# Performance work log

Measured on AMD Instinct MI355X. Metric: run time of the kernel, lower is better.

The kernel has to match this reference:

```python
import jax, jax.numpy as jnp
import numpy as np


def _mlp1(x, W, b):
    return jax.nn.relu(x @ W + b)


def _forward(battle_x, side_x, user_x, moveset_feat, movepool_feat, lookup_move_feat,
             lookup_move_mask, lastberry, lastberry_mask, items, abilities, types_x,
             tera_types_x, opt_moves, move_mask, can_tera, switch_mask,
             W_item, b_item, W_ab, b_ab, W_ms, b_ms, W_user, b_user,
             W_mo1, b_mo1, W_mo2, b_mo2, W_so1, b_so1, W_so2, b_so2,
             active_idx, switch_idx):
    B = battle_x.shape[0]
    # --- user block (vectorized over [B, 2 sides, 6 team members]) ---
    ms = _mlp1(moveset_feat, W_ms, b_ms)                    # [B,2,6,4,128]
    pool = _mlp1(movepool_feat, W_ms, b_ms).mean(axis=-2)   # [B,2,6,128] mean over move pool
    move_set_x = jnp.maximum(ms.max(axis=-2), pool)         # max over [4 slots + pool-mean]
    item_x = _mlp1(items, W_item, b_item).mean(axis=-2)     # [B,2,6,128]
    ability_x = _mlp1(abilities, W_ab, b_ab).mean(axis=-2)  # [B,2,6,128]
    # optional lookup slots: mask*relu(Wx+b) == zero vector when absent
    lk = _mlp1(lookup_move_feat, W_ms, b_ms) * lookup_move_mask[..., None]  # [B,2,6,5,128]
    berry = _mlp1(lastberry, W_item, b_item) * lastberry_mask[..., None]    # [B,2,6,128]
    lk_flat = lk.reshape(B, 2, 6, 5 * 128)
    u_in = jnp.concatenate([user_x, lk_flat, berry, move_set_x, item_x, ability_x,
                            types_x, tera_types_x], axis=-1)                # [B,2,6,1281]
    u = _mlp1(u_in, W_user, b_user)                                         # [B,2,6,512]
    # --- side block ---
    active = jnp.take_along_axis(u, active_idx[:, :, None, None], axis=2)[:, :, 0]  # [B,2,512]
    side_out = jnp.concatenate([side_x, active, u.max(axis=2)], axis=-1)    # [B,2,1041]
    battle_full = jnp.concatenate([battle_x, side_out[:, 0], side_out[:, 1]], axis=-1)  # [B,2091]
    D = battle_full.shape[-1]
    # --- move options: 4 moves x tera in {0,1} ---
    bt = jnp.broadcast_to(battle_full[:, None, None, :], (B, 4, 2, D))
    mv = jnp.broadcast_to(opt_moves[:, :, None, :], (B, 4, 2, 128))
    tera = jnp.broadcast_to(jnp.arange(2, dtype=battle_x.dtype)[None, None, :, None], (B, 4, 2, 1))
    xm = jnp.concatenate([bt, mv, tera], axis=-1)                           # [B,4,2,2220]
    mlogit = (_mlp1(xm, W_mo1, b_mo1) @ W_mo2 + b_mo2)[..., 0]              # [B,4,2]
    tera_ok = jnp.stack([jnp.ones_like(can_tera), can_tera], axis=-1)       # [B,2]
    mvalid = move_mask[:, :, None] * tera_ok[:, None, :]
    mlogit = jnp.where(mvalid > 0, mlogit, -jnp.inf).reshape(B, 8)
    # --- switch options ---
    sw = jnp.take_along_axis(u[:, 0], switch_idx[:, :, None], axis=1)       # [B,6,512]
    xs = jnp.concatenate([jnp.broadcast_to(battle_full[:, None, :], (B, 6, D)), sw], axis=-1)
    slogit = (_mlp1(xs, W_so1, b_so1) @ W_so2 + b_so2)[..., 0]              # [B,6]
    slogit = jnp.where(switch_mask > 0, slogit, -jnp.inf)
    return jnp.concatenate([mlogit, slogit], axis=-1)                       # [B,14]


def setup_inputs() -> dict:
    key = jax.random.key(0)
    ks = jax.random.split(key, 40)
    B = 512
    f32 = jnp.float32
    n = lambda k, s, sc=1.0: jax.random.normal(k, s, f32) * sc
    bern = lambda k, s, p: (jax.random.uniform(k, s) < p).astype(f32)
    inp = {
        'battle_x': n(ks[0], (B, 9)),
        'side_x': n(ks[1], (B, 2, 17)),
        'user_x': n(ks[2], (B, 2, 6, 89)),
        'moveset_feat': n(ks[3], (B, 2, 6, 4, 516)),
        'movepool_feat': n(ks[4], (B, 2, 6, 8, 516)),
        'lookup_move_feat': n(ks[5], (B, 2, 6, 5, 516)),
        'lookup_move_mask': bern(ks[6], (B, 2, 6, 5), 0.5),
        'lastberry': n(ks[7], (B, 2, 6, 256)),
        'lastberry_mask': bern(ks[8], (B, 2, 6), 0.5),
        'items': n(ks[9], (B, 2, 6, 2, 256)),
        'abilities': n(ks[10], (B, 2, 6, 2, 256)),
        'types_x': bern(ks[11], (B, 2, 6, 20), 0.1),
        'tera_types_x': bern(ks[12], (B, 2, 6, 20), 0.1),
        'opt_moves': n(ks[13], (B, 4, 128)),
        'move_mask': bern(ks[14], (B, 4), 0.9),
        'can_tera': bern(ks[15], (B,), 0.5),
        'switch_mask': bern(ks[16], (B, 6), 0.8),
        'W_item': n(ks[17], (256, 128), 0.05), 'b_item': n(ks[18], (128,), 0.05),
        'W_ab': n(ks[19], (256, 128), 0.05), 'b_ab': n(ks[20], (128,), 0.05),
        'W_ms': n(ks[21], (516, 128), 0.05), 'b_ms': n(ks[22], (128,), 0.05),
        'W_user': n(ks[23], (1281, 512), 0.02), 'b_user': n(ks[24], (512,), 0.02),
        'W_mo1': n(ks[25], (2220, 512), 0.02), 'b_mo1': n(ks[26], (512,), 0.02),
        'W_mo2': n(ks[27], (512, 1), 0.05), 'b_mo2': n(ks[28], (1,), 0.05),
        'W_so1': n(ks[29], (2603, 512), 0.02), 'b_so1': n(ks[30], (512,), 0.02),
        'W_so2': n(ks[31], (512, 1), 0.05), 'b_so2': n(ks[32], (1,), 0.05),
        'active_idx': jax.random.randint(ks[33], (B, 2), 0, 6),
        'switch_idx': jax.random.randint(ks[34], (B, 6), 0, 6),
    }
    return inp


def reference(battle_x, side_x, user_x, moveset_feat, movepool_feat, lookup_move_feat,
              lookup_move_mask, lastberry, lastberry_mask, items, abilities, types_x,
              tera_types_x, opt_moves, move_mask, can_tera, switch_mask,
              W_item, b_item, W_ab, b_ab, W_ms, b_ms, W_user, b_user,
              W_mo1, b_mo1, W_mo2, b_mo2, W_so1, b_so1, W_so2, b_so2,
              active_idx, switch_idx):
    return _forward(battle_x, side_x, user_x, moveset_feat, movepool_feat, lookup_move_feat,
                    lookup_move_mask, lastberry, lastberry_mask, items, abilities, types_x,
                    tera_types_x, opt_moves, move_mask, can_tera, switch_mask,
                    W_item, b_item, W_ab, b_ab, W_ms, b_ms, W_user, b_user,
                    W_mo1, b_mo1, W_mo2, b_mo2, W_so1, b_so1, W_so2, b_so2,
                    active_idx, switch_idx)
```

## Files before the change

kernel.cpp:

```cpp
#include <hip/hip_runtime.h>
#include <math.h>

#define BATCH 512
#define NEG_BIG (-3.0e38f)

typedef __attribute__((ext_vector_type(8))) short short8;
typedef __attribute__((ext_vector_type(4))) float floatx4;

__device__ inline unsigned pk2(float lo, float hi) {
    return __builtin_amdgcn_perm(__float_as_uint(hi), __float_as_uint(lo), 0x07060302u);
}
__device__ inline short8 cvt8(float4 a, float4 b) {
    union { unsigned u[4]; short8 s; } r;
    r.u[0] = pk2(a.x, a.y); r.u[1] = pk2(a.z, a.w);
    r.u[2] = pk2(b.x, b.y); r.u[3] = pk2(b.z, b.w);
    return r.s;
}
__device__ inline short f2bf(float f) {
    unsigned u = __float_as_uint(f);
    u += 0x7FFFu + ((u >> 16) & 1u);
    return (short)(u >> 16);
}
__device__ inline float bf2f(short s) {
    return __uint_as_float(((unsigned)(unsigned short)s) << 16);
}

__device__ inline void wprep_body(
    const float* __restrict__ W, int K, int N,
    short* __restrict__ Wt, int KP, int k_off,
    int lid, int kbt, float (*tile)[33])
{
    const int kb = (lid % kbt) * 32, nb = (lid / kbt) * 32;
    const int c = threadIdx.x & 31, r0 = threadIdx.x >> 5;
    #pragma unroll
    for (int i = 0; i < 4; ++i) {
        const int r = r0 + i * 8;
        const int k = kb + r;
        tile[r][c] = (k < K) ? W[(size_t)k * N + nb + c] : 0.f;
    }
    __syncthreads();
    #pragma unroll
    for (int i = 0; i < 4; ++i) {
        const int n = nb + r0 + i * 8;
        Wt[(size_t)n * KP + k_off + kb + c] = f2bf(tile[c][r0 + i * 8]);
    }
}

__global__ __launch_bounds__(256) void k_wprep_all(
    const float* __restrict__ W_ms, const float* __restrict__ W_item,
    const float* __restrict__ W_ab, const float* __restrict__ W_user,
    const float* __restrict__ W_mo1, const float* __restrict__ W_so1,
    short* __restrict__ Wt_pre, short* __restrict__ Wt_user,
    short* __restrict__ Wt_mo, short* __restrict__ Wt_mv,
    short* __restrict__ Wt_so, short* __restrict__ Wt_sw)
{
    __shared__ float tile[32][33];
    const int l = blockIdx.x;
    if      (l < 68)   wprep_body(W_ms,   516,  128, Wt_pre,  1056, 0,   l,        17, tile);
    else if (l < 100)  wprep_body(W_item, 256,  128, Wt_pre,  1056, 544, l - 68,   8,  tile);
    else if (l < 132)  wprep_body(W_ab,   256,  128, Wt_pre,  1056, 800, l - 100,  8,  tile);
    else if (l < 788)  wprep_body(W_user, 1281, 512, Wt_user, 1312, 0,   l - 132,  41, tile);
    else if (l < 1844) wprep_body(W_mo1,  2091, 512, Wt_mo,   2112, 0,   l - 788,  66, tile);
    else if (l < 1908) wprep_body(W_mo1 + (size_t)2091 * 512, 128, 512, Wt_mv, 128, 0, l - 1844, 4, tile);
    else if (l < 2964) wprep_body(W_so1,  2091, 512, Wt_so,   2112, 0,   l - 1908, 66, tile);
    else               wprep_body(W_so1 + (size_t)2091 * 512, 512, 512, Wt_sw, 512, 0, l - 2964, 16, tile);
}

#define STRA 552
#define SIOFF 18768
#define STRI 264
#define ZEROE 528

__device__ inline void stage4(short* S, int e, float4 v) {
    uint2 wv; wv.x = pk2(v.x, v.y); wv.y = pk2(v.z, v.w);
    *(uint2*)(S + e) = wv;
}

__global__ __launch_bounds__(256, 3) void k_pre_gemm(
    const float* __restrict__ moveset, const float* __restrict__ movepool,
    const float* __restrict__ lookup,  const float* __restrict__ items,
    const float* __restrict__ lastberry, const float* __restrict__ abilities,
    const float* __restrict__ lookup_mask, const float* __restrict__ berry_mask,
    const float* __restrict__ user_x, const float* __restrict__ types_x,
    const float* __restrict__ tera_types,
    const short* __restrict__ Wt,
    const float* __restrict__ b_ms, const float* __restrict__ b_item,
    const float* __restrict__ b_ab,
    short* __restrict__ u_in)
{
    __shared__ __align__(16) short S[21408];
    const int t = threadIdx.x;
    const int bsu0 = blockIdx.x * 2;

    {
        #pragma unroll
        for (int j = 0; j < 2; ++j) {
            const int i = t + j * 256;
            if (i < 476) {
                const int rr = i / 14, p = i - rr * 14;
                *(unsigned*)(S + rr * STRA + 516 + p * 2) = 0u;
            }
        }

        const float4* msrc = (const float4*)(moveset + (size_t)bsu0 * 4 * 516);
        const float4* psrc = (const float4*)(movepool + (size_t)bsu0 * 8 * 516);
        const float4* lsrc = (const float4*)(lookup + (size_t)bsu0 * 5 * 516);
        const float4* isrc = (const float4*)(items + (size_t)bsu0 * 2 * 256);
        const float4* bsrc = (const float4*)(lastberry + (size_t)bsu0 * 256);
        const float4* asrc = (const float4*)(abilities + (size_t)bsu0 * 2 * 256);

        float4 rm[5], rp[9], rl[6], rit, rlb, rab;
        #pragma unroll
        for (int j = 0; j < 5; ++j) {
            int i = t + j * 256; if (i > 1031) i = 1031;
            rm[j] = msrc[i];
        }
        #pragma unroll
        for (int j = 0; j < 9; ++j) {
            int i = t + j * 256; if (i > 2063) i = 2063;
            rp[j] = psrc[i];
        }
        #pragma unroll
        for (int j = 0; j < 6; ++j) {
            int i = t + j * 256; if (i > 1289) i = 1289;
            rl[j] = lsrc[i];
        }
        rit = isrc[t];
        rlb = bsrc[t & 127];
        rab = asrc[t];

        __builtin_amdgcn_sched_barrier(0);

        #pragma unroll
        for (int j = 0; j < 5; ++j) {
            int i = t + j * 256; if (i > 1031) i = 1031;
            const int g = i / 129, jj = i - g * 129;
            stage4(S, ((g >> 2) * 17 + (g & 3)) * STRA + jj * 4, rm[j]);
        }
        #pragma unroll
        for (int j = 0; j < 9; ++j) {
            int i = t + j * 256; if (i > 2063) i = 2063;
            const int g = i / 129, jj = i - g * 129;
            stage4(S, ((g >> 3) * 17 + 4 + (g & 7)) * STRA + jj * 4, rp[j]);
        }
        #pragma unroll
        for (int j = 0; j < 6; ++j) {
            int i = t + j * 256; if (i > 1289) i = 1289;
            const int g = i / 129, jj = i - g * 129;
            const int b = g / 5, r = g - b * 5;
            stage4(S, (b * 17 + 12 + r) * STRA + jj * 4, rl[j]);
        }
        {
            const int g = t >> 6, j = t & 63;
            stage4(S, SIOFF + ((g >> 1) * 5 + (g & 1)) * STRI + j * 4, rit);
        }
        {
            const int i = t & 127, g = i >> 6, j = i & 63;
            stage4(S, SIOFF + (g * 5 + 2) * STRI + j * 4, rlb);
        }
        {
            const int g = t >> 6, j = t & 63;
            stage4(S, SIOFF + ((g >> 1) * 5 + 3 + (g & 1)) * STRI + j * 4, rab);
        }
    }
    __syncthreads();

    const int lane = t & 63, w = t >> 6;
    const int m = lane & 15, q = lane >> 4;

    int t2base = ZEROE, t2lo = 1, t2hi = 0;
    {
        int jj = m, b = 0;
        if (m >= 6 && m < 12) { b = 1; jj = m - 6; }
        if (m < 12) {
            if (jj == 0)      { t2base = (b * 17 + 16) * STRA;             t2lo = 0;  t2hi = 16; }
            else if (jj <= 2) { t2base = SIOFF + (b * 5 + (jj - 1)) * STRI; t2lo = 17; t2hi = 24; }
            else if (jj == 3) { t2base = SIOFF + (b * 5 + 2) * STRI;        t2lo = 17; t2hi = 24; }
            else              { t2base = SIOFF + (b * 5 + 3 + (jj - 4)) * STRI; t2lo = 25; t2hi = 32; }
        }
    }
    const short* bp0 = Wt + (size_t)(w * 32 + m) * 1056 + q * 8;
    const short* bp1 = bp0 + (size_t)16 * 1056;

    floatx4 acc[3][2];
    #pragma unroll
    for (int i = 0; i < 3; ++i) {
        acc[i][0] = (floatx4){0.f, 0.f, 0.f, 0.f};
        acc[i][1] = (floatx4){0.f, 0.f, 0.f, 0.f};
    }

    short8 B0[4], B1[4];
    #pragma unroll
    for (int d = 0; d < 4; ++d) {
        B0[d] = *(const short8*)(bp0 + d * 32);
        B1[d] = *(const short8*)(bp1 + d * 32);
    }
    const int aoff = q * 8;

    #pragma unroll
    for (int s = 0; s <= 16; ++s) {
        const int k0 = s * 32 + aoff;
        short8 a0 = *(const short8*)(S + m * STRA + k0);
        short8 a1 = *(const short8*)(S + (17 + m) * STRA + k0);
        const int e2 = (s >= t2lo && s <= t2hi) ? t2base + (s - t2lo) * 32 + aoff : ZEROE;
        short8 a2 = *(const short8*)(S + e2);
        acc[0][0] = __builtin_amdgcn_mfma_f32_16x16x32_bf16(a0, B0[s & 3], acc[0][0], 0, 0, 0);
        acc[0][1] = __builtin_amdgcn_mfma_f32_16x16x32_bf16(a0, B1[s & 3], acc[0][1], 0, 0, 0);
        acc[1][0] = __builtin_amdgcn_mfma_f32_16x16x32_bf16(a1, B0[s & 3], acc[1][0], 0, 0, 0);
        acc[1][1] = __builtin_amdgcn_mfma_f32_16x16x32_bf16(a1, B1[s & 3], acc[1][1], 0, 0, 0);
        acc[2][0] = __builtin_amdgcn_mfma_f32_16x16x32_bf16(a2, B0[s & 3], acc[2][0], 0, 0, 0);
        acc[2][1] = __builtin_amdgcn_mfma_f32_16x16x32_bf16(a2, B1[s & 3], acc[2][1], 0, 0, 0);
        if (s + 4 <= 32) {
            B0[s & 3] = *(const short8*)(bp0 + (s + 4) * 32);
            B1[s & 3] = *(const short8*)(bp1 + (s + 4) * 32);
        }
    }
    #pragma unroll
    for (int s = 17; s <= 32; ++s) {
        const int e2 = (s >= t2lo && s <= t2hi) ? t2base + (s - t2lo) * 32 + aoff : ZEROE;
        short8 a2 = *(const short8*)(S + e2);
        acc[2][0] = __builtin_amdgcn_mfma_f32_16x16x32_bf16(a2, B0[s & 3], acc[2][0], 0, 0, 0);
        acc[2][1] = __builtin_amdgcn_mfma_f32_16x16x32_bf16(a2, B1[s & 3], acc[2][1], 0, 0, 0);
        if (s + 4 <= 32) {
            B0[s & 3] = *(const short8*)(bp0 + (s + 4) * 32);
            B1[s & 3] = *(const short8*)(bp1 + (s + 4) * 32);
        }
    }

    __syncthreads();
    float* ec = (float*)S;

    #pragma unroll
    for (int nt = 0; nt < 2; ++nt) {
        const int col = w * 32 + nt * 16 + m;
        #pragma unroll
        for (int r = 0; r < 4; ++r) {
            const int row = q * 4 + r;
            ec[col * 49 + row]      = acc[0][nt][r];
            ec[col * 49 + 24 + row] = acc[1][nt][r];
            if (row < 6)            ec[col * 49 + 16 + row]            = acc[2][nt][r];
            else if (row < 12)      ec[col * 49 + 24 + 16 + (row - 6)] = acc[2][nt][r];
        }
    }
    __syncthreads();
    {
        const int c  = t & 127;
        const int bi = t >> 7;
        const int bsu = bsu0 + bi;
        const float* v = &ec[c * 49 + bi * 24];
        short* __restrict__ orow = u_in + (size_t)bsu * 1312;
        const float bms = b_ms[c], bit = b_item[c], bab = b_ab[c];
        float msx = 0.f;
        #pragma unroll
        for (int r = 0; r < 4; ++r) msx = fmaxf(msx, v[r] + bms);
        float pool = 0.f;
        #pragma unroll
        for (int r = 4; r < 12; ++r) pool += fmaxf(v[r] + bms, 0.f);
        pool *= 0.125f;
        orow[857 + c] = f2bf(fmaxf(msx, pool));
        #pragma unroll
        for (int sl = 0; sl < 5; ++sl) {
            const float mask = lookup_mask[bsu * 5 + sl];
            orow[89 + sl * 128 + c] = f2bf(fmaxf(v[12 + sl] + bms, 0.f) * mask);
        }
        orow[985 + c]  = f2bf(0.5f * (fmaxf(v[17] + bit, 0.f) + fmaxf(v[18] + bit, 0.f)));
        orow[729 + c]  = f2bf(fmaxf(v[19] + bit, 0.f) * berry_mask[bsu]);
        orow[1113 + c] = f2bf(0.5f * (fmaxf(v[20] + bab, 0.f) + fmaxf(v[21] + bab, 0.f)));
        if (c < 89) orow[c] = f2bf(user_x[(size_t)bsu * 89 + c]);
        if (c < 20) {
            orow[1241 + c] = f2bf(types_x[bsu * 20 + c]);
            orow[1261 + c] = f2bf(tera_types[bsu * 20 + c]);
        }
        if (c < 31) orow[1281 + c] = 0;
    }
}

template<int AMODE, bool ABF16, bool RELU, bool HASBIAS, bool OBF16>
__global__ __launch_bounds__(256, 3) void k_gemm(
    const void* __restrict__ Av, int strideA,
    const void* __restrict__ gbasev, const int* __restrict__ gidx,
    const short* __restrict__ Wt, int KP,
    const float* __restrict__ bias,
    void* __restrict__ Cv, size_t partStride, int ksteps)
{
    const int t = threadIdx.x, lane = t & 63, w = t >> 6;
    const int m = lane & 15, q = lane >> 4;
    const int bid = blockIdx.y * gridDim.x + blockIdx.x;
    const int mb = (bid / gridDim.y) * 32;
    const int nb = (bid % gridDim.y) * 128 + w * 32;
    const int z = blockIdx.z;
    const int koff = z * ksteps * 32;

    const short* aps[2]; const float* apf[2];
    #pragma unroll
    for (int i = 0; i < 2; ++i) {
        const int row = mb + i * 16 + m;
        size_t roff;
        if (AMODE == 0) roff = (size_t)row * strideA;
        else {
            const int bb = row / 6, j = row - bb * 6;
            roff = ((size_t)bb * 12 + gidx[bb * 6 + j]) * 512;
        }
        if (ABF16) aps[i] = (const short*)Av + roff + koff + q * 8;
        else       apf[i] = (const float*)Av + roff + koff + q * 8;
        if (AMODE == 1) aps[i] = (const short*)gbasev + roff + koff + q * 8;
    }
    const short* bp0 = Wt + (size_t)(nb + m) * KP + koff + q * 8;
    const short* bp1 = bp0 + (size_t)16 * KP;

    floatx4 acc[2][2];
    #pragma unroll
    for (int i = 0; i < 2; ++i) {
        acc[i][0] = (floatx4){0.f, 0.f, 0.f, 0.f};
        acc[i][1] = (floatx4){0.f, 0.f, 0.f, 0.f};
    }

    short8 Ab[4][2];
    float4 Af[4][2][2];
    short8 B0b[4], B1b[4];
    #pragma unroll
    for (int d = 0; d < 4; ++d) {
        #pragma unroll
        for (int i = 0; i < 2; ++i) {
            if (ABF16) Ab[d][i] = *(const short8*)(aps[i] + d * 32);
            else {
                Af[d][i][0] = *(const float4*)(apf[i] + d * 32);
                Af[d][i][1] = *(const float4*)(apf[i] + d * 32 + 4);
            }
        }
        B0b[d] = *(const short8*)(bp0 + d * 32);
        B1b[d] = *(const short8*)(bp1 + d * 32);
    }

    int s = 0;
    for (; s + 4 < ksteps; s += 4) {
        #pragma unroll
        for (int d = 0; d < 4; ++d) {
            #pragma unroll
            for (int i = 0; i < 2; ++i) {
                const short8 av = ABF16 ? Ab[d][i] : cvt8(Af[d][i][0], Af[d][i][1]);
                acc[i][0] = __builtin_amdgcn_mfma_f32_16x16x32_bf16(av, B0b[d], acc[i][0], 0, 0, 0);
                acc[i][1] = __builtin_amdgcn_mfma_f32_16x16x32_bf16(av, B1b[d], acc[i][1], 0, 0, 0);
            }
            int ns = s + d + 4; if (ns > ksteps - 1) ns = ksteps - 1;
            const int o = ns * 32;
            #pragma unroll
            for (int i = 0; i < 2; ++i) {
                if (ABF16) Ab[d][i] = *(const short8*)(aps[i] + o);
                else {
                    Af[d][i][0] = *(const float4*)(apf[i] + o);
                    Af[d][i][1] = *(const float4*)(apf[i] + o + 4);
                }
            }
            B0b[d] = *(const short8*)(bp0 + o);
            B1b[d] = *(const short8*)(bp1 + o);
        }
    }
    #pragma unroll
    for (int d = 0; d < 4; ++d) {
        if (s + d < ksteps) {
            #pragma unroll
            for (int i = 0; i < 2; ++i) {
                const short8 av = ABF16 ? Ab[d][i] : cvt8(Af[d][i][0], Af[d][i][1]);
                acc[i][0] = __builtin_amdgcn_mfma_f32_16x16x32_bf16(av, B0b[d], acc[i][0], 0, 0, 0);
                acc[i][1] = __builtin_amdgcn_mfma_f32_16x16x32_bf16(av, B1b[d], acc[i][1], 0, 0, 0);
            }
        }
    }

    const float bb0 = (HASBIAS && z == 0) ? bias[nb + m] : 0.f;
    const float bb1 = (HASBIAS && z == 0) ? bias[nb + 16 + m] : 0.f;
    #pragma unroll
    for (int i = 0; i < 2; ++i) {
        #pragma unroll
        for (int r = 0; r < 4; ++r) {
            const int row = mb + i * 16 + q * 4 + r;
            float v0 = acc[i][0][r] + bb0;
            float v1 = acc[i][1][r] + bb1;
            if (RELU) { v0 = fmaxf(v0, 0.f); v1 = fmaxf(v1, 0.f); }
            if (OBF16) {
                short* C = (short*)Cv + z * partStride;
                C[(size_t)row * 512 + nb + m]      = f2bf(v0);
                C[(size_t)row * 512 + nb + 16 + m] = f2bf(v1);
            } else {
                float* C = (float*)Cv + z * partStride;
                C[(size_t)row * 512 + nb + m]      = v0;
                C[(size_t)row * 512 + nb + 16 + m] = v1;
            }
        }
    }
}

__global__ __launch_bounds__(256) void k_battle(
    const float* __restrict__ battle_x, const float* __restrict__ side_x,
    const short* __restrict__ u, const int* __restrict__ active_idx,
    short* __restrict__ bfb)
{
    const int b = blockIdx.x;
    const int t = threadIdx.x;
    short* __restrict__ o = bfb + (size_t)b * 2112;
    if (t < 9) o[t] = f2bf(battle_x[b * 9 + t]);
    if (t < 21) o[2091 + t] = 0;
    for (int s = 0; s < 2; ++s) {
        const short* __restrict__ us = u + (size_t)(b * 2 + s) * 6 * 512;
        const int act = active_idx[b * 2 + s];
        if (t < 17) o[9 + s * 1041 + t] = f2bf(side_x[(b * 2 + s) * 17 + t]);
        for (int c = t; c < 512; c += 256) {
            float mx = bf2f(us[c]);
            #pragma unroll
            for (int uu = 1; uu < 6; ++uu) mx = fmaxf(mx, bf2f(us[uu * 512 + c]));
            o[9 + s * 1041 + 17 + c]       = us[act * 512 + c];
            o[9 + s * 1041 + 17 + 512 + c] = f2bf(mx);
        }
    }
}

__global__ __launch_bounds__(512) void k_epi_mo(
    const float* __restrict__ C_mo, size_t partStride, int nparts,
    const float* __restrict__ D_mv,
    const float* __restrict__ W1, const float* __restrict__ W2,
    const float* __restrict__ b2,
    const float* __restrict__ move_mask, const float* __restrict__ can_tera,
    float* __restrict__ out)
{
    __shared__ float red[8][8];
    const int b = blockIdx.x, t = threadIdx.x;
    float h = 0.f;
    for (int p = 0; p < nparts; ++p) h += C_mo[p * partStride + (size_t)b * 512 + t];
    const float wt = W1[(size_t)2219 * 512 + t];
    const float w2 = W2[t];
    float dm[4];
    #pragma unroll
    for (int m = 0; m < 4; ++m) dm[m] = D_mv[((size_t)b * 4 + m) * 512 + t];
    const int lane = t & 63, wid = t >> 6;
    #pragma unroll
    for (int m = 0; m < 4; ++m) {
        #pragma unroll
        for (int tt = 0; tt < 2; ++tt) {
            float hv = fmaxf(h + dm[m] + (tt ? wt : 0.f), 0.f);
            float v = hv * w2;
            #pragma unroll
            for (int off = 32; off > 0; off >>= 1) v += __shfl_down(v, off);
            if (lane == 0) red[m * 2 + tt][wid] = v;
        }
    }
    __syncthreads();
    if (t < 8) {
        float s = 0.f;
        #pragma unroll
        for (int ww = 0; ww < 8; ++ww) s += red[t][ww];
        s += b2[0];
        const int m = t >> 1, tt = t & 1;
        const float ok = move_mask[b * 4 + m] * (tt ? can_tera[b] : 1.f);
        out[b * 14 + t] = (ok > 0.f) ? s : NEG_BIG;
    }
}

__global__ __launch_bounds__(512) void k_epi_sw(
    const float* __restrict__ C_so, size_t partStride, int nparts,
    const float* __restrict__ D_sw,
    const float* __restrict__ W2, const float* __restrict__ b2,
    const float* __restrict__ switch_mask, float* __restrict__ out)
{
    __shared__ float red[6][8];
    const int b = blockIdx.x, t = threadIdx.x;
    float h = 0.f;
    for (int p = 0; p < nparts; ++p) h += C_so[p * partStride + (size_t)b * 512 + t];
    const float w2 = W2[t];
    const int lane = t & 63, wid = t >> 6;
    #pragma unroll
    for (int j = 0; j < 6; ++j) {
        float hv = fmaxf(h + D_sw[((size_t)b * 6 + j) * 512 + t], 0.f);
        float v = hv * w2;
        #pragma unroll
        for (int off = 32; off > 0; off >>= 1) v += __shfl_down(v, off);
        if (lane == 0) red[j][wid] = v;
    }
    __syncthreads();
    if (t < 6) {
        float s = 0.f;
        #pragma unroll
        for (int ww = 0; ww < 8; ++ww) s += red[t][ww];
        s += b2[0];
        out[b * 14 + 8 + t] = (switch_mask[b * 6 + t] > 0.f) ? s : NEG_BIG;
    }
}

extern "C" void kernel_launch(void* const* d_in, const int* in_sizes, int n_in,
                              void* d_out, int out_size, void* d_ws, size_t ws_size,
                              hipStream_t stream) {
    const float* battle_x    = (const float*)d_in[0];
    const float* side_x      = (const float*)d_in[1];
    const float* user_x      = (const float*)d_in[2];
    const float* moveset     = (const float*)d_in[3];
    const float* movepool    = (const float*)d_in[4];
    const float* lookup      = (const float*)d_in[5];
    const float* lookup_mask = (const float*)d_in[6];
    const float* lastberry   = (const float*)d_in[7];
    const float* berry_mask  = (const float*)d_in[8];
    const float* items       = (const float*)d_in[9];
    const float* abilities   = (const float*)d_in[10];
    const float* types_x     = (const float*)d_in[11];
    const float* tera_types  = (const float*)d_in[12];
    const float* opt_moves   = (const float*)d_in[13];
    const float* move_mask   = (const float*)d_in[14];
    const float* can_tera    = (const float*)d_in[15];
    const float* switch_mask = (const float*)d_in[16];
    const float* W_item = (const float*)d_in[17];
    const float* b_item = (const float*)d_in[18];
    const float* W_ab   = (const float*)d_in[19];
    const float* b_ab   = (const float*)d_in[20];
    const float* W_ms   = (const float*)d_in[21];
    const float* b_ms   = (const float*)d_in[22];
    const float* W_user = (const float*)d_in[23];
    const float* b_user = (const float*)d_in[24];
    const float* W_mo1  = (const float*)d_in[25];
    const float* b_mo1  = (const float*)d_in[26];
    const float* W_mo2  = (const float*)d_in[27];
    const float* b_mo2  = (const float*)d_in[28];
    const float* W_so1  = (const float*)d_in[29];
    const float* b_so1  = (const float*)d_in[30];
    const float* W_so2  = (const float*)d_in[31];
    const float* b_so2  = (const float*)d_in[32];
    const int* active_idx = (const int*)d_in[33];
    const int* switch_idx = (const int*)d_in[34];
    float* out = (float*)d_out;

    char* base = (char*)d_ws;
    size_t off = 0;
    short* u_in = (short*)(base + off); off += (size_t)6144 * 1312 * 2;
    short* u    = (short*)(base + off); off += (size_t)6144 * 512 * 2;
    short* bfb  = (short*)(base + off); off += (size_t)512 * 2112 * 2;
    float* C_mo = (float*)(base + off); off += (size_t)6 * 512 * 512 * 4;
    float* C_so = (float*)(base + off); off += (size_t)6 * 512 * 512 * 4;
    float* D_mv = (float*)(base + off); off += (size_t)2048 * 512 * 4;
    float* D_sw = (float*)(base + off); off += (size_t)3072 * 512 * 4;
    short* Wt_pre  = (short*)(base + off); off += (size_t)128 * 1056 * 2;
    short* Wt_user = (short*)(base + off); off += (size_t)512 * 1312 * 2;
    short* Wt_mo   = (short*)(base + off); off += (size_t)512 * 2112 * 2;
    short* Wt_so   = (short*)(base + off); off += (size_t)512 * 2112 * 2;
    short* Wt_mv   = (short*)(base + off); off += (size_t)512 * 128 * 2;
    short* Wt_sw   = (short*)(base + off); off += (size_t)512 * 512 * 2;

    k_wprep_all<<<3220, 256, 0, stream>>>(W_ms, W_item, W_ab, W_user, W_mo1, W_so1,
                                          Wt_pre, Wt_user, Wt_mo, Wt_mv, Wt_so, Wt_sw);

    k_pre_gemm<<<3072, 256, 0, stream>>>(moveset, movepool, lookup, items, lastberry,
                                         abilities, lookup_mask, berry_mask,
                                         user_x, types_x, tera_types,
                                         Wt_pre, b_ms, b_item, b_ab, u_in);
    k_gemm<0, true, true, true, true><<<dim3(192, 4, 1), 256, 0, stream>>>(
        u_in, 1312, nullptr, nullptr, Wt_user, 1312, b_user, u, 0, 41);
    k_battle<<<BATCH, 256, 0, stream>>>(battle_x, side_x, u, active_idx, bfb);
    k_gemm<0, true, false, true, false><<<dim3(16, 4, 6), 256, 0, stream>>>(
        bfb, 2112, nullptr, nullptr, Wt_mo, 2112, b_mo1, C_mo, (size_t)512 * 512, 11);
    k_gemm<0, false, false, false, false><<<dim3(64, 4, 1), 256, 0, stream>>>(
        opt_moves, 128, nullptr, nullptr, Wt_mv, 128, nullptr, D_mv, 0, 4);
    k_gemm<0, true, false, true, false><<<dim3(16, 4, 6), 256, 0, stream>>>(
        bfb, 2112, nullptr, nullptr, Wt_so, 2112, b_so1, C_so, (size_t)512 * 512, 11);
    k_gemm<1, true, false, false, false><<<dim3(96, 4, 1), 256, 0, stream>>>(
        nullptr, 0, u, switch_idx, Wt_sw, 512, nullptr, D_sw, 0, 16);
    k_epi_mo<<<BATCH, 512, 0, stream>>>(C_mo, (size_t)512 * 512, 6, D_mv, W_mo1,
                                        W_mo2, b_mo2, move_mask, can_tera, out);
    k_epi_sw<<<BATCH, 512, 0, stream>>>(C_so, (size_t)512 * 512, 6, D_sw,
                                        W_so2, b_so2, switch_mask, out);
}
```

Measured before the change: 471.7 us.

## Stage pre-GEMM inputs via direct global-to-LDS loads, one user per block

The pre-GEMM kernel now loads fp32 move, pool, lookup, item and ability features straight into shared memory with global_load_lds, skipping the register round trip. Conversion to bf16 moves into the MFMA loop at LDS read time. Each block now handles one team member instead of two, so the grid doubles and per-block accumulators shrink. The cost is twice the weight-fragment loads per unit of work, redundant conversions, and more blocks. The direct-to-LDS path may also behave differently in latency.

```diff
diff --git a/kernel.cpp b/kernel.cpp
--- a/kernel.cpp
+++ b/kernel.cpp
@@ -23,6 +23,12 @@
 }
 __device__ inline float bf2f(short s) {
     return __uint_as_float(((unsigned)(unsigned short)s) << 16);
+}
+
+typedef const __attribute__((address_space(1))) unsigned GU32;
+typedef __attribute__((address_space(3))) unsigned LU32;
+__device__ inline void gload16(const float* g, float* l) {
+    __builtin_amdgcn_global_load_lds((GU32*)g, (LU32*)l, 16, 0, 0);
 }
 
 __device__ inline void wprep_body(
@@ -66,15 +72,10 @@
     else               wprep_body(W_so1 + (size_t)2091 * 512, 512, 512, Wt_sw, 512, 0, l - 2964, 16, tile);
 }
 
-#define STRA 552
-#define SIOFF 18768
-#define STRI 264
-#define ZEROE 528
-
-__device__ inline void stage4(short* S, int e, float4 v) {
-    uint2 wv; wv.x = pk2(v.x, v.y); wv.y = pk2(v.z, v.w);
-    *(uint2*)(S + e) = wv;
-}
+#define ASTR 548
+#define IOFF 9316
+#define ISTR 260
+#define ZF   516
 
 __global__ __launch_bounds__(256, 3) void k_pre_gemm(
     const float* __restrict__ moveset, const float* __restrict__ movepool,
@@ -88,103 +89,55 @@
     const float* __restrict__ b_ab,
     short* __restrict__ u_in)
 {
-    __shared__ __align__(16) short S[21408];
+    __shared__ __align__(16) float Sf[10616];
     const int t = threadIdx.x;
-    const int bsu0 = blockIdx.x * 2;
+    const int bsu = blockIdx.x;
+    const int lane = t & 63, w = t >> 6;
 
     {
-        #pragma unroll
-        for (int j = 0; j < 2; ++j) {
-            const int i = t + j * 256;
-            if (i < 476) {
-                const int rr = i / 14, p = i - rr * 14;
-                *(unsigned*)(S + rr * STRA + 516 + p * 2) = 0u;
-            }
-        }
-
-        const float4* msrc = (const float4*)(moveset + (size_t)bsu0 * 4 * 516);
-        const float4* psrc = (const float4*)(movepool + (size_t)bsu0 * 8 * 516);
-        const float4* lsrc = (const float4*)(lookup + (size_t)bsu0 * 5 * 516);
-        const float4* isrc = (const float4*)(items + (size_t)bsu0 * 2 * 256);
-        const float4* bsrc = (const float4*)(lastberry + (size_t)bsu0 * 256);
-        const float4* asrc = (const float4*)(abilities + (size_t)bsu0 * 2 * 256);
-
-        float4 rm[5], rp[9], rl[6], rit, rlb, rab;
-        #pragma unroll
-        for (int j = 0; j < 5; ++j) {
-            int i = t + j * 256; if (i > 1031) i = 1031;
-            rm[j] = msrc[i];
-        }
-        #pragma unroll
-        for (int j = 0; j < 9; ++j) {
-            int i = t + j * 256; if (i > 2063) i = 2063;
-            rp[j] = psrc[i];
-        }
-        #pragma unroll
-        for (int j = 0; j < 6; ++j) {
-            int i = t + j * 256; if (i > 1289) i = 1289;
-            rl[j] = lsrc[i];
-        }
-        rit = isrc[t];
-        rlb = bsrc[t & 127];
-        rab = asrc[t];
-
-        __builtin_amdgcn_sched_barrier(0);
-
-        #pragma unroll
-        for (int j = 0; j < 5; ++j) {
-            int i = t + j * 256; if (i > 1031) i = 1031;
-            const int g = i / 129, jj = i - g * 129;
-            stage4(S, ((g >> 2) * 17 + (g & 3)) * STRA + jj * 4, rm[j]);
-        }
-        #pragma unroll
-        for (int j = 0; j < 9; ++j) {
-            int i = t + j * 256; if (i > 2063) i = 2063;
-            const int g = i / 129, jj = i - g * 129;
-            stage4(S, ((g >> 3) * 17 + 4 + (g & 7)) * STRA + jj * 4, rp[j]);
-        }
-        #pragma unroll
-        for (int j = 0; j < 6; ++j) {
-            int i = t + j * 256; if (i > 1289) i = 1289;
-            const int g = i / 129, jj = i - g * 129;
-            const int b = g / 5, r = g - b * 5;
-            stage4(S, (b * 17 + 12 + r) * STRA + jj * 4, rl[j]);
-        }
-        {
-            const int g = t >> 6, j = t & 63;
-            stage4(S, SIOFF + ((g >> 1) * 5 + (g & 1)) * STRI + j * 4, rit);
-        }
-        {
-            const int i = t & 127, g = i >> 6, j = i & 63;
-            stage4(S, SIOFF + (g * 5 + 2) * STRI + j * 4, rlb);
-        }
-        {
-            const int g = t >> 6, j = t & 63;
-            stage4(S, SIOFF + ((g >> 1) * 5 + 3 + (g & 1)) * STRI + j * 4, rab);
+        const int i0 = t, i1 = t + 256;
+        if (i0 < 544) Sf[(i0 >> 5) * ASTR + 516 + (i0 & 31)] = 0.f;
+        if (i1 < 544) Sf[(i1 >> 5) * ASTR + 516 + (i1 & 31)] = 0.f;
+    }
+
+    for (int r = w; r < 17; r += 4) {
+        const float* src = (r < 4)  ? moveset  + ((size_t)bsu * 4 + r) * 516
+                         : (r < 12) ? movepool + ((size_t)bsu * 8 + (r - 4)) * 516
+                                    : lookup   + ((size_t)bsu * 5 + (r - 12)) * 516;
+        float* dst = Sf + r * ASTR;
+        gload16(src + lane * 4, dst);
+        gload16(src + 256 + lane * 4, dst + 256);
+        if (lane == 0) gload16(src + 512, dst + 512);
+    }
+    {
+        float* If = Sf + IOFF;
+        if (w == 1) {
+            gload16(items     + ((size_t)bsu * 2 + 0) * 256 + lane * 4, If + 0 * ISTR);
+            gload16(abilities + ((size_t)bsu * 2 + 0) * 256 + lane * 4, If + 3 * ISTR);
+        } else if (w == 2) {
+            gload16(items     + ((size_t)bsu * 2 + 1) * 256 + lane * 4, If + 1 * ISTR);
+            gload16(abilities + ((size_t)bsu * 2 + 1) * 256 + lane * 4, If + 4 * ISTR);
+        } else if (w == 3) {
+            gload16(lastberry + (size_t)bsu * 256 + lane * 4, If + 2 * ISTR);
         }
     }
     __syncthreads();
 
-    const int lane = t & 63, w = t >> 6;
     const int m = lane & 15, q = lane >> 4;
-
-    int t2base = ZEROE, t2lo = 1, t2hi = 0;
-    {
-        int jj = m, b = 0;
-        if (m >= 6 && m < 12) { b = 1; jj = m - 6; }
-        if (m < 12) {
-            if (jj == 0)      { t2base = (b * 17 + 16) * STRA;             t2lo = 0;  t2hi = 16; }
-            else if (jj <= 2) { t2base = SIOFF + (b * 5 + (jj - 1)) * STRI; t2lo = 17; t2hi = 24; }
-            else if (jj == 3) { t2base = SIOFF + (b * 5 + 2) * STRI;        t2lo = 17; t2hi = 24; }
-            else              { t2base = SIOFF + (b * 5 + 3 + (jj - 4)) * STRI; t2lo = 25; t2hi = 32; }
-        }
-    }
+    const int aoff = q * 8;
+
+    int t2base = ZF, t2lo = 1, t2hi = 0;
+    if (m == 0)      { t2base = 16 * ASTR;              t2lo = 0;  t2hi = 16; }
+    else if (m <= 2) { t2base = IOFF + (m - 1) * ISTR;  t2lo = 17; t2hi = 24; }
+    else if (m == 3) { t2base = IOFF + 2 * ISTR;        t2lo = 17; t2hi = 24; }
+    else if (m <= 5) { t2base = IOFF + (m - 1) * ISTR;  t2lo = 25; t2hi = 32; }
+
     const short* bp0 = Wt + (size_t)(w * 32 + m) * 1056 + q * 8;
     const short* bp1 = bp0 + (size_t)16 * 1056;
 
-    floatx4 acc[3][2];
-    #pragma unroll
-    for (int i = 0; i < 3; ++i) {
+    floatx4 acc[2][2];
+    #pragma unroll
+    for (int i = 0; i < 2; ++i) {
         acc[i][0] = (floatx4){0.f, 0.f, 0.f, 0.f};
         acc[i][1] = (floatx4){0.f, 0.f, 0.f, 0.f};
     }
@@ -195,21 +148,17 @@
         B0[d] = *(const short8*)(bp0 + d * 32);
         B1[d] = *(const short8*)(bp1 + d * 32);
     }
-    const int aoff = q * 8;
 
     #pragma unroll
     for (int s = 0; s <= 16; ++s) {
-        const int k0 = s * 32 + aoff;
-        short8 a0 = *(const short8*)(S + m * STRA + k0);
-        short8 a1 = *(const short8*)(S + (17 + m) * STRA + k0);
-        const int e2 = (s >= t2lo && s <= t2hi) ? t2base + (s - t2lo) * 32 + aoff : ZEROE;
-        short8 a2 = *(const short8*)(S + e2);
+        const int k0 = m * ASTR + s * 32 + aoff;
+        short8 a0 = cvt8(*(const float4*)(Sf + k0), *(const float4*)(Sf + k0 + 4));
+        const int e2 = (s >= t2lo && s <= t2hi) ? t2base + (s - t2lo) * 32 + aoff : ZF;
+        short8 a2 = cvt8(*(const float4*)(Sf + e2), *(const float4*)(Sf + e2 + 4));
         acc[0][0] = __builtin_amdgcn_mfma_f32_16x16x32_bf16(a0, B0[s & 3], acc[0][0], 0, 0, 0);
         acc[0][1] = __builtin_amdgcn_mfma_f32_16x16x32_bf16(a0, B1[s & 3], acc[0][1], 0, 0, 0);
-        acc[1][0] = __builtin_amdgcn_mfma_f32_16x16x32_bf16(a1, B0[s & 3], acc[1][0], 0, 0, 0);
-        acc[1][1] = __builtin_amdgcn_mfma_f32_16x16x32_bf16(a1, B1[s & 3], acc[1][1], 0, 0, 0);
-        acc[2][0] = __builtin_amdgcn_mfma_f32_16x16x32_bf16(a2, B0[s & 3], acc[2][0], 0, 0, 0);
-        acc[2][1] = __builtin_amdgcn_mfma_f32_16x16x32_bf16(a2, B1[s & 3], acc[2][1], 0, 0, 0);
+        acc[1][0] = __builtin_amdgcn_mfma_f32_16x16x32_bf16(a2, B0[s & 3], acc[1][0], 0, 0, 0);
+        acc[1][1] = __builtin_amdgcn_mfma_f32_16x16x32_bf16(a2, B1[s & 3], acc[1][1], 0, 0, 0);
         if (s + 4 <= 32) {
             B0[s & 3] = *(const short8*)(bp0 + (s + 4) * 32);
             B1[s & 3] = *(const short8*)(bp1 + (s + 4) * 32);
@@ -217,10 +166,10 @@
     }
     #pragma unroll
     for (int s = 17; s <= 32; ++s) {
-        const int e2 = (s >= t2lo && s <= t2hi) ? t2base + (s - t2lo) * 32 + aoff : ZEROE;
-        short8 a2 = *(const short8*)(S + e2);
-        acc[2][0] = __builtin_amdgcn_mfma_f32_16x16x32_bf16(a2, B0[s & 3], acc[2][0], 0, 0, 0);
-        acc[2][1] = __builtin_amdgcn_mfma_f32_16x16x32_bf16(a2, B1[s & 3], acc[2][1], 0, 0, 0);
+        const int e2 = (s >= t2lo && s <= t2hi) ? t2base + (s - t2lo) * 32 + aoff : ZF;
+        short8 a2 = cvt8(*(const float4*)(Sf + e2), *(const float4*)(Sf + e2 + 4));
+        acc[1][0] = __builtin_amdgcn_mfma_f32_16x16x32_bf16(a2, B0[s & 3], acc[1][0], 0, 0, 0);
+        acc[1][1] = __builtin_amdgcn_mfma_f32_16x16x32_bf16(a2, B1[s & 3], acc[1][1], 0, 0, 0);
         if (s + 4 <= 32) {
             B0[s & 3] = *(const short8*)(bp0 + (s + 4) * 32);
             B1[s & 3] = *(const short8*)(bp1 + (s + 4) * 32);
@@ -228,7 +177,7 @@
     }
 
     __syncthreads();
-    float* ec = (float*)S;
+    float* ec = Sf;
 
     #pragma unroll
     for (int nt = 0; nt < 2; ++nt) {
@@ -236,18 +185,14 @@
         #pragma unroll
         for (int r = 0; r < 4; ++r) {
             const int row = q * 4 + r;
-            ec[col * 49 + row]      = acc[0][nt][r];
-            ec[col * 49 + 24 + row] = acc[1][nt][r];
-            if (row < 6)            ec[col * 49 + 16 + row]            = acc[2][nt][r];
-            else if (row < 12)      ec[col * 49 + 24 + 16 + (row - 6)] = acc[2][nt][r];
+            ec[col * 25 + row] = acc[0][nt][r];
+            if (row < 6) ec[col * 25 + 16 + row] = acc[1][nt][r];
         }
     }
     __syncthreads();
-    {
-        const int c  = t & 127;
-        const int bi = t >> 7;
-        const int bsu = bsu0 + bi;
-        const float* v = &ec[c * 49 + bi * 24];
+    if (t < 128) {
+        const int c = t;
+        const float* v = &ec[c * 25];
         short* __restrict__ orow = u_in + (size_t)bsu * 1312;
         const float bms = b_ms[c], bit = b_item[c], bab = b_ab[c];
         float msx = 0.f;
@@ -545,7 +490,7 @@
     k_wprep_all<<<3220, 256, 0, stream>>>(W_ms, W_item, W_ab, W_user, W_mo1, W_so1,
                                           Wt_pre, Wt_user, Wt_mo, Wt_mv, Wt_so, Wt_sw);
 
-    k_pre_gemm<<<3072, 256, 0, stream>>>(moveset, movepool, lookup, items, lastberry,
+    k_pre_gemm<<<6144, 256, 0, stream>>>(moveset, movepool, lookup, items, lastberry,
                                          abilities, lookup_mask, berry_mask,
                                          user_x, types_x, tera_types,
                                          Wt_pre, b_ms, b_item, b_ab, u_in);
```

Measured after the change: 535.6 us. 1.14x slower.

## Use 512 threads in pre-GEMM kernel, one N-subtile per wave

Applied to the files above, without the earlier changes.

Doubles the k_pre_gemm block to 512 threads (8 waves). Each wave now computes a single 16-column N tile instead of two, which halves its accumulators and B registers. The staging loads change from a register-batched prefetch behind a sched_barrier to direct load-then-store loops spread over more threads, and the pad zeroing moves after the staging stores. The aim is more waves in flight to hide global-load latency. In exchange, each wave has less instruction-level parallelism, A-fragment LDS reads are repeated across twice as many waves, and half the threads sit idle in the epilogue.

```diff
diff --git a/kernel.cpp b/kernel.cpp
--- a/kernel.cpp
+++ b/kernel.cpp
@@ -76,7 +76,7 @@
     *(uint2*)(S + e) = wv;
 }
 
-__global__ __launch_bounds__(256, 3) void k_pre_gemm(
+__global__ __launch_bounds__(512, 6) void k_pre_gemm(
     const float* __restrict__ moveset, const float* __restrict__ movepool,
     const float* __restrict__ lookup,  const float* __restrict__ items,
     const float* __restrict__ lastberry, const float* __restrict__ abilities,
@@ -93,15 +93,6 @@
     const int bsu0 = blockIdx.x * 2;
 
     {
-        #pragma unroll
-        for (int j = 0; j < 2; ++j) {
-            const int i = t + j * 256;
-            if (i < 476) {
-                const int rr = i / 14, p = i - rr * 14;
-                *(unsigned*)(S + rr * STRA + 516 + p * 2) = 0u;
-            }
-        }
-
         const float4* msrc = (const float4*)(moveset + (size_t)bsu0 * 4 * 516);
         const float4* psrc = (const float4*)(movepool + (size_t)bsu0 * 8 * 516);
         const float4* lsrc = (const float4*)(lookup + (size_t)bsu0 * 5 * 516);
@@ -109,58 +100,40 @@
         const float4* bsrc = (const float4*)(lastberry + (size_t)bsu0 * 256);
         const float4* asrc = (const float4*)(abilities + (size_t)bsu0 * 2 * 256);
 
-        float4 rm[5], rp[9], rl[6], rit, rlb, rab;
+        #pragma unroll
+        for (int j = 0; j < 3; ++j) {
+            int i = t + j * 512; if (i > 1031) i = 1031;
+            const int g = i / 129, jj = i - g * 129;
+            stage4(S, ((g >> 2) * 17 + (g & 3)) * STRA + jj * 4, msrc[i]);
+        }
         #pragma unroll
         for (int j = 0; j < 5; ++j) {
-            int i = t + j * 256; if (i > 1031) i = 1031;
-            rm[j] = msrc[i];
-        }
-        #pragma unroll
-        for (int j = 0; j < 9; ++j) {
-            int i = t + j * 256; if (i > 2063) i = 2063;
-            rp[j] = psrc[i];
-        }
-        #pragma unroll
-        for (int j = 0; j < 6; ++j) {
-            int i = t + j * 256; if (i > 1289) i = 1289;
-            rl[j] = lsrc[i];
-        }
-        rit = isrc[t];
-        rlb = bsrc[t & 127];
-        rab = asrc[t];
-
-        __builtin_amdgcn_sched_barrier(0);
-
-        #pragma unroll
-        for (int j = 0; j < 5; ++j) {
-            int i = t + j * 256; if (i > 1031) i = 1031;
+            int i = t + j * 512; if (i > 2063) i = 2063;
             const int g = i / 129, jj = i - g * 129;
-            stage4(S, ((g >> 2) * 17 + (g & 3)) * STRA + jj * 4, rm[j]);
-        }
-        #pragma unroll
-        for (int j = 0; j < 9; ++j) {
-            int i = t + j * 256; if (i > 2063) i = 2063;
-            const int g = i / 129, jj = i - g * 129;
-            stage4(S, ((g >> 3) * 17 + 4 + (g & 7)) * STRA + jj * 4, rp[j]);
-        }
-        #pragma unroll
-        for (int j = 0; j < 6; ++j) {
-            int i = t + j * 256; if (i > 1289) i = 1289;
+            stage4(S, ((g >> 3) * 17 + 4 + (g & 7)) * STRA + jj * 4, psrc[i]);
+        }
+        #pragma unroll
+        for (int j = 0; j < 3; ++j) {
+            int i = t + j * 512; if (i > 1289) i = 1289;
             const int g = i / 129, jj = i - g * 129;
             const int b = g / 5, r = g - b * 5;
-            stage4(S, (b * 17 + 12 + r) * STRA + jj * 4, rl[j]);
+            stage4(S, (b * 17 + 12 + r) * STRA + jj * 4, lsrc[i]);
         }
         {
-            const int g = t >> 6, j = t & 63;
-            stage4(S, SIOFF + ((g >> 1) * 5 + (g & 1)) * STRI + j * 4, rit);
+            const int i = t & 255, g = i >> 6, j = i & 63;
+            stage4(S, SIOFF + ((g >> 1) * 5 + (g & 1)) * STRI + j * 4, isrc[i]);
         }
         {
             const int i = t & 127, g = i >> 6, j = i & 63;
-            stage4(S, SIOFF + (g * 5 + 2) * STRI + j * 4, rlb);
+            stage4(S, SIOFF + (g * 5 + 2) * STRI + j * 4, bsrc[i]);
         }
         {
-            const int g = t >> 6, j = t & 63;
-            stage4(S, SIOFF + ((g >> 1) * 5 + 3 + (g & 1)) * STRI + j * 4, rab);
+            const int i = t & 255, g = i >> 6, j = i & 63;
+            stage4(S, SIOFF + ((g >> 1) * 5 + 3 + (g & 1)) * STRI + j * 4, asrc[i]);
+        }
+        if (t < 476) {
+            const int rr = t / 14, p = t - rr * 14;
+            *(unsigned*)(S + rr * STRA + 516 + p * 2) = 0u;
         }
     }
     __syncthreads();
@@ -179,22 +152,15 @@
             else              { t2base = SIOFF + (b * 5 + 3 + (jj - 4)) * STRI; t2lo = 25; t2hi = 32; }
         }
     }
-    const short* bp0 = Wt + (size_t)(w * 32 + m) * 1056 + q * 8;
-    const short* bp1 = bp0 + (size_t)16 * 1056;
-
-    floatx4 acc[3][2];
-    #pragma unroll
-    for (int i = 0; i < 3; ++i) {
-        acc[i][0] = (floatx4){0.f, 0.f, 0.f, 0.f};
-        acc[i][1] = (floatx4){0.f, 0.f, 0.f, 0.f};
-    }
-
-    short8 B0[4], B1[4];
-    #pragma unroll
-    for (int d = 0; d < 4; ++d) {
-        B0[d] = *(const short8*)(bp0 + d * 32);
-        B1[d] = *(const short8*)(bp1 + d * 32);
-    }
+    const short* bp0 = Wt + (size_t)(w * 16 + m) * 1056 + q * 8;
+
+    floatx4 acc[3];
+    #pragma unroll
+    for (int i = 0; i < 3; ++i) acc[i] = (floatx4){0.f, 0.f, 0.f, 0.f};
+
+    short8 B0[4];
+    #pragma unroll
+    for (int d = 0; d < 4; ++d) B0[d] = *(const short8*)(bp0 + d * 32);
     const int aoff = q * 8;
 
     #pragma unroll
@@ -204,46 +170,39 @@
         short8 a1 = *(const short8*)(S + (17 + m) * STRA + k0);
         const int e2 = (s >= t2lo && s <= t2hi) ? t2base + (s - t2lo) * 32 + aoff : ZEROE;
         short8 a2 = *(const short8*)(S + e2);
-        acc[0][0] = __builtin_amdgcn_mfma_f32_16x16x32_bf16(a0, B0[s & 3], acc[0][0], 0, 0, 0);
-        acc[0][1] = __builtin_amdgcn_mfma_f32_16x16x32_bf16(a0, B1[s & 3], acc[0][1], 0, 0, 0);
-        acc[1][0] = __builtin_amdgcn_mfma_f32_16x16x32_bf16(a1, B0[s & 3], acc[1][0], 0, 0, 0);
-        acc[1][1] = __builtin_amdgcn_mfma_f32_16x16x32_bf16(a1, B1[s & 3], acc[1][1], 0, 0, 0);
-        acc[2][0] = __builtin_amdgcn_mfma_f32_16x16x32_bf16(a2, B0[s & 3], acc[2][0], 0, 0, 0);
-        acc[2][1] = __builtin_amdgcn_mfma_f32_16x16x32_bf16(a2, B1[s & 3], acc[2][1], 0, 0, 0);
+        acc[0] = __builtin_amdgcn_mfma_f32_16x16x32_bf16(a0, B0[s & 3], acc[0], 0, 0, 0);
+        acc[1] = __builtin_amdgcn_mfma_f32_16x16x32_bf16(a1, B0[s & 3], acc[1], 0, 0, 0);
+        acc[2] = __builtin_amdgcn_mfma_f32_16x16x32_bf16(a2, B0[s & 3], acc[2], 0, 0, 0);
         if (s + 4 <= 32) {
             B0[s & 3] = *(const short8*)(bp0 + (s + 4) * 32);
-            B1[s & 3] = *(const short8*)(bp1 + (s + 4) * 32);
         }
     }
     #pragma unroll
     for (int s = 17; s <= 32; ++s) {
         const int e2 = (s >= t2lo && s <= t2hi) ? t2base + (s - t2lo) * 32 + aoff : ZEROE;
         short8 a2 = *(const short8*)(S + e2);
-        acc[2][0] = __builtin_amdgcn_mfma_f32_16x16x32_bf16(a2, B0[s & 3], acc[2][0], 0, 0, 0);
-        acc[2][1] = __builtin_amdgcn_mfma_f32_16x16x32_bf16(a2, B1[s & 3], acc[2][1], 0, 0, 0);
+        acc[2] = __builtin_amdgcn_mfma_f32_16x16x32_bf16(a2, B0[s & 3], acc[2], 0, 0, 0);
         if (s + 4 <= 32) {
             B0[s & 3] = *(const short8*)(bp0 + (s + 4) * 32);
-            B1[s & 3] = *(const short8*)(bp1 + (s + 4) * 32);
         }
     }
 
     __syncthreads();
     float* ec = (float*)S;
 
-    #pragma unroll
-    for (int nt = 0; nt < 2; ++nt) {
-        const int col = w * 32 + nt * 16 + m;
+    {
+        const int col = w * 16 + m;
         #pragma unroll
         for (int r = 0; r < 4; ++r) {
             const int row = q * 4 + r;
-            ec[col * 49 + row]      = acc[0][nt][r];
-            ec[col * 49 + 24 + row] = acc[1][nt][r];
-            if (row < 6)            ec[col * 49 + 16 + row]            = acc[2][nt][r];
-            else if (row < 12)      ec[col * 49 + 24 + 16 + (row - 6)] = acc[2][nt][r];
+            ec[col * 49 + row]      = acc[0][r];
+            ec[col * 49 + 24 + row] = acc[1][r];
+            if (row < 6)            ec[col * 49 + 16 + row]            = acc[2][r];
+            else if (row < 12)      ec[col * 49 + 24 + 16 + (row - 6)] = acc[2][r];
         }
     }
     __syncthreads();
-    {
+    if (t < 256) {
         const int c  = t & 127;
         const int bi = t >> 7;
         const int bsu = bsu0 + bi;
@@ -545,7 +504,7 @@
     k_wprep_all<<<3220, 256, 0, stream>>>(W_ms, W_item, W_ab, W_user, W_mo1, W_so1,
                                           Wt_pre, Wt_user, Wt_mo, Wt_mv, Wt_so, Wt_sw);
 
-    k_pre_gemm<<<3072, 256, 0, stream>>>(moveset, movepool, lookup, items, lastberry,
+    k_pre_gemm<<<3072, 512, 0, stream>>>(moveset, movepool, lookup, items, lastberry,
                                          abilities, lookup_mask, berry_mask,
                                          user_x, types_x, tera_types,
                                          Wt_pre, b_ms, b_item, b_ab, u_in);
```

New measurement: 478.7 us. No clear change (+1.5%).
